# Kernel tuning notes

Hardware: AMD Instinct MI355X
Metric: run time of the kernel (lower is better)

Reference implementation:

```python
import jax, jax.numpy as jnp
import numpy as np

B, N, C, D, H = 256, 1024, 100, 256, 16
QD = D // H              # per-head dim
CLIP = 10.0              # logit_clipping
NEG = -1000000000.0      # masked_fill value in torch source


def setup_inputs() -> dict:
    key = jax.random.key(0)
    ks = jax.random.split(key, 12)
    s = 0.05
    inp = {
        "depot_embedding": jax.random.normal(ks[0], (B, 1, D), jnp.float32),
        "cluster_embedding": jax.random.normal(ks[1], (B, C + 1, D), jnp.float32),
        "current_embedding": jax.random.normal(ks[2], (B, 1, D), jnp.float32),
        "node_embeddings": jax.random.normal(ks[3], (B, N, D), jnp.float32),
        # visited-node / other-cluster / visited-cluster masks (bool)
        "mask": jax.random.bernoulli(ks[4], 0.2, (B, 1, N)),
        "cluster_mask": jax.random.bernoulli(ks[5], 0.5, (B, 1, N)),
        "visited_cluster_mask": jax.random.bernoulli(ks[6], 0.3, (B, 1, C + 1)).at[:, :, C].set(False),
        # Linear weights stored as (in, out) so y = x @ W
        "Wq": jax.random.normal(ks[7], (3 * D, D), jnp.float32) * s,
        "Wk": jax.random.normal(ks[8], (D, D), jnp.float32) * s,
        "Wv": jax.random.normal(ks[9], (D, D), jnp.float32) * s,
        "Wks": jax.random.normal(ks[10], (D, D), jnp.float32) * s,
        "Wo": jax.random.normal(ks[11], (D, D), jnp.float32) * s,
    }
    return inp


def _unvisited_mean(emb, m):
    # emb: [B,N,D], m: [B,1,N] bool -> masked mean over unvisited nodes [B,1,D]
    keep = (~m).astype(emb.dtype).transpose(0, 2, 1)          # [B,N,1]
    denom = jnp.clip(keep.sum(axis=1, keepdims=True), 1.0)    # [B,1,1]
    return (emb * keep).sum(axis=1, keepdims=True) / denom


def reference(depot_embedding, cluster_embedding, current_embedding,
              node_embeddings, mask, cluster_mask, visited_cluster_mask,
              Wq, Wk, Wv, Wks, Wo):
    b = node_embeddings.shape[0]
    # context query: [unvisited-mean, current, depot] -> [B,1,3D]
    uv = _unvisited_mean(node_embeddings, mask)
    context = jnp.concatenate([uv, current_embedding, depot_embedding], axis=-1)
    q = context @ Wq                    # [B,1,D]
    k = cluster_embedding @ Wk          # [B,C+1,D]
    v = cluster_embedding @ Wv
    prob_k = cluster_embedding @ Wks

    # visited-cluster mask; depot (col 0) only allowed once all real clusters visited
    vm = visited_cluster_mask[:, 0, :]                        # [B,C+1]
    all_real_visited = jnp.all(vm[:, 1:], axis=1)
    vm = vm.at[:, 0].set(~all_real_visited)

    # multi-head glimpse attention
    qh = q.reshape(b, 1, H, QD).transpose(0, 2, 1, 3)         # [B,H,1,QD]
    kh = k.reshape(b, -1, H, QD).transpose(0, 2, 1, 3)        # [B,H,C+1,QD]
    vh = v.reshape(b, -1, H, QD).transpose(0, 2, 1, 3)
    scores = jnp.einsum('bhqe,bhke->bhqk', qh, kh) / jnp.sqrt(jnp.float32(QD))
    scores = jnp.where(vm[:, None, None, :], NEG, scores)
    attn = jax.nn.softmax(scores, axis=-1)
    glimpse = jnp.einsum('bhqk,bhke->bhqe', attn, vh)
    glimpse = glimpse.transpose(0, 2, 1, 3).reshape(b, 1, D) @ Wo   # [B,1,D]

    # single-head pointer logits over clusters
    logits = jnp.einsum('bqd,bkd->bqk', glimpse, prob_k)[:, 0, :] / jnp.sqrt(jnp.float32(D))
    logits = jnp.tanh(logits) * CLIP
    logits = jnp.where(vm, NEG, logits)
    local_log_p = jax.nn.log_softmax(logits, axis=1)          # [B,C+1]

    # greedy cluster selection + gather
    selected_cluster = jnp.argmax(local_log_p, axis=1)        # [B] int
    sel_emb = jnp.take_along_axis(cluster_embedding,
                                  selected_cluster[:, None, None], axis=1)  # [B,1,D]

    uvc = _unvisited_mean(node_embeddings, mask | cluster_mask)
    init_aug = jnp.concatenate([uvc, current_embedding, sel_emb, depot_embedding], axis=-1)  # [B,1,4D]
    init_guidance_emb = sel_emb
    init_guidance = selected_cluster
    clu_prob = local_log_p
    return init_aug, init_guidance_emb, init_guidance, clu_prob
```

## Files before the change

### kernel.cpp

```cpp
#include <hip/hip_runtime.h>
#include <math.h>

#define B_SZ 256
#define N_SZ 1024
#define NCL  101
#define D_SZ 256
#define NH   16
#define APAD 260
#define NEGV (-1000000000.0f)


__device__ __forceinline__ bool mask_at(const void* p, long idx, int mode) {
  if (mode == 0) return ((const int*)p)[idx] != 0;
  if (mode == 1) return ((const unsigned char*)p)[idx] != 0;
  return ((const float*)p)[idx] != 0.0f;
}

__global__ void detect_mode_kernel(const unsigned int* m, int* flag) {
  if (threadIdx.x == 0 && blockIdx.x == 0) {
    bool isf = false, nonbin = false;
    for (int i = 0; i < 256; ++i) {
      unsigned int v = m[i];
      if (v == 0x3F800000u) isf = true;
      else if (v > 1u) nonbin = true;
    }
    *flag = isf ? 2 : (nonbin ? 1 : 0);
  }
}

__global__ __launch_bounds__(256) void mean_partial_kernel(
    const float* __restrict__ node, const void* __restrict__ mask,
    const void* __restrict__ cmask, const int* __restrict__ flag,
    int* __restrict__ counts, float* __restrict__ partials) {
  const int bs = blockIdx.x;
  const int b = bs >> 3, s = bs & 7;
  const int tid = threadIdx.x;
  const int mode = *flag;
  const int r0 = s * 128;
  __shared__ float f1[128], f2[128];
  __shared__ int wc1[2], wc2[2];
  __shared__ float red[4][D_SZ];

  int c1 = 0, c2 = 0;
  if (tid < 128) {
    const long idx = (long)b * N_SZ + r0 + tid;
    const bool m1 = mask_at(mask, idx, mode);
    const bool m2 = mask_at(cmask, idx, mode);
    const int k1 = m1 ? 0 : 1;
    const int k2 = (m1 || m2) ? 0 : 1;
    f1[tid] = (float)k1; f2[tid] = (float)k2;
    c1 = k1; c2 = k2;
  }
  #pragma unroll
  for (int off = 32; off > 0; off >>= 1) {
    c1 += __shfl_down(c1, off);
    c2 += __shfl_down(c2, off);
  }
  if (tid == 0)  { wc1[0] = c1; wc2[0] = c2; }
  if (tid == 64) { wc1[1] = c1; wc2[1] = c2; }
  __syncthreads();
  if (tid == 0) {
    counts[bs * 2 + 0] = wc1[0] + wc1[1];
    counts[bs * 2 + 1] = wc2[0] + wc2[1];
  }

  const int rg = tid >> 6;
  const int c4 = (tid & 63) << 2;
  const float* base = node + ((size_t)b * N_SZ + r0) * D_SZ + c4;
  float4 s1 = {0.f,0.f,0.f,0.f}, s2 = {0.f,0.f,0.f,0.f};
  #pragma unroll 8
  for (int k = 0; k < 32; ++k) {
    const int row = rg * 32 + k;
    const float4 x = *(const float4*)(base + (size_t)row * D_SZ);
    const float k1 = f1[row], k2 = f2[row];
    s1.x = fmaf(x.x, k1, s1.x); s1.y = fmaf(x.y, k1, s1.y);
    s1.z = fmaf(x.z, k1, s1.z); s1.w = fmaf(x.w, k1, s1.w);
    s2.x = fmaf(x.x, k2, s2.x); s2.y = fmaf(x.y, k2, s2.y);
    s2.z = fmaf(x.z, k2, s2.z); s2.w = fmaf(x.w, k2, s2.w);
  }
  *(float4*)&red[rg][c4] = s1;
  __syncthreads();
  {
    float t = red[0][tid] + red[1][tid] + red[2][tid] + red[3][tid];
    partials[((size_t)bs * 2 + 0) * D_SZ + tid] = t;
  }
  __syncthreads();
  *(float4*)&red[rg][c4] = s2;
  __syncthreads();
  {
    float t = red[0][tid] + red[1][tid] + red[2][tid] + red[3][tid];
    partials[((size_t)bs * 2 + 1) * D_SZ + tid] = t;
  }
}

struct __align__(16) SMem {
  float At[16][APAD];
  union { float tT[NH][APAD]; float uB[NH][APAD]; } tu;
  float sc[NH][104];
  float ctx[3 * D_SZ];
  float q[D_SZ];
  float g[D_SZ];
  float go[D_SZ];
  float w[D_SZ];
  float logits[104];
  int   vm[104];
  float lse_s;
  int   sel_s;
};

__global__ __launch_bounds__(256) void main_kernel(
    const float* __restrict__ depot, const float* __restrict__ cluster,
    const float* __restrict__ current, const void* __restrict__ vcm,
    const int* __restrict__ flag,
    const float* __restrict__ Wq, const float* __restrict__ Wk,
    const float* __restrict__ Wv, const float* __restrict__ Wks,
    const float* __restrict__ Wo,
    const int* __restrict__ counts, const float* __restrict__ partials,
    float* __restrict__ out) {
  __shared__ SMem S;
  const int b = blockIdx.x, tid = threadIdx.x;
  const int mode = *flag;
  const float* Ab = cluster + (size_t)b * NCL * D_SZ;

  float uvv = 0.f, uvcv = 0.f;
  #pragma unroll
  for (int s = 0; s < 8; ++s) {
    uvv  += partials[((size_t)(b * 8 + s) * 2 + 0) * D_SZ + tid];
    uvcv += partials[((size_t)(b * 8 + s) * 2 + 1) * D_SZ + tid];
  }
  int t1 = 0, t2 = 0;
  #pragma unroll
  for (int s = 0; s < 8; ++s) {
    t1 += counts[(b * 8 + s) * 2 + 0];
    t2 += counts[(b * 8 + s) * 2 + 1];
  }
  const float uvcval = uvcv / fmaxf((float)t2, 1.0f);

  if (tid < NCL) S.vm[tid] = mask_at(vcm, (long)b * NCL + tid, mode) ? 1 : 0;
  S.ctx[tid]       = uvv / fmaxf((float)t1, 1.0f);
  S.ctx[256 + tid] = current[b * D_SZ + tid];
  S.ctx[512 + tid] = depot[b * D_SZ + tid];
  __syncthreads();
  if (tid == 0) {
    int all1 = 1;
    for (int c = 1; c < NCL; ++c) all1 &= S.vm[c];
    S.vm[0] = all1 ? 0 : 1;
  }

  {
    float a0 = 0.f, a1 = 0.f, a2 = 0.f, a3 = 0.f;
    for (int i = 0; i < 3 * D_SZ; i += 4) {
      a0 = fmaf(S.ctx[i + 0], Wq[(size_t)(i + 0) * D_SZ + tid], a0);
      a1 = fmaf(S.ctx[i + 1], Wq[(size_t)(i + 1) * D_SZ + tid], a1);
      a2 = fmaf(S.ctx[i + 2], Wq[(size_t)(i + 2) * D_SZ + tid], a2);
      a3 = fmaf(S.ctx[i + 3], Wq[(size_t)(i + 3) * D_SZ + tid], a3);
    }
    S.q[tid] = (a0 + a1) + (a2 + a3);
  }
  __syncthreads();

  {
    const int h = tid & 15, i0 = tid >> 4;
    float qh[16];
    #pragma unroll
    for (int e = 0; e < 16; ++e) qh[e] = S.q[h * 16 + e];
    for (int k = 0; k < 16; ++k) {
      const int i = i0 + 16 * k;
      const float* wr = Wk + (size_t)i * D_SZ + h * 16;
      float acc = 0.f;
      #pragma unroll
      for (int e = 0; e < 16; ++e) acc = fmaf(wr[e], qh[e], acc);
      S.tu.tT[h][i] = acc;
    }
  }
  __syncthreads();

  for (int ch = 0; ch < 7; ++ch) {
    const int r0 = ch * 16;
    for (int x = tid; x < 16 * 64; x += 256) {
      const int r = x >> 6, cc = (x & 63) << 2;
      if (r0 + r < NCL) {
        const float4 v = *(const float4*)(Ab + (size_t)(r0 + r) * D_SZ + cc);
        *(float4*)&S.At[r][cc] = v;
      }
    }
    __syncthreads();
    {
      const int h = tid >> 4, cl = tid & 15, c = r0 + cl;
      float p0 = 0.f, p1 = 0.f, p2 = 0.f, p3 = 0.f;
      for (int i = 0; i < D_SZ; i += 4) {
        const float4 av = *(const float4*)&S.At[cl][i];
        const float4 tv = *(const float4*)&S.tu.tT[h][i];
        p0 = fmaf(av.x, tv.x, p0);
        p1 = fmaf(av.y, tv.y, p1);
        p2 = fmaf(av.z, tv.z, p2);
        p3 = fmaf(av.w, tv.w, p3);
      }
      if (c < NCL) {
        float sv = 0.25f * ((p0 + p1) + (p2 + p3));
        if (S.vm[c]) sv = NEGV;
        S.sc[h][c] = sv;
      }
    }
    __syncthreads();
  }

  {
    const int h = tid >> 4, j = tid & 15;
    float m = -3.0e38f;
    for (int c = j; c < NCL; c += 16) m = fmaxf(m, S.sc[h][c]);
    #pragma unroll
    for (int off = 8; off > 0; off >>= 1) m = fmaxf(m, __shfl_xor(m, off, 16));
    float ssum = 0.f;
    for (int c = j; c < NCL; c += 16) {
      const float e = expf(S.sc[h][c] - m);
      S.sc[h][c] = e;
      ssum += e;
    }
    #pragma unroll
    for (int off = 8; off > 0; off >>= 1) ssum += __shfl_xor(ssum, off, 16);
    const float inv = 1.0f / ssum;
    for (int c = j; c < NCL; c += 16) S.sc[h][c] *= inv;
  }
  __syncthreads();

  {
    float u[16];
    #pragma unroll
    for (int h = 0; h < 16; ++h) u[h] = 0.f;
    for (int ch = 0; ch < 7; ++ch) {
      const int r0 = ch * 16;
      for (int x = tid; x < 16 * 64; x += 256) {
        const int r = x >> 6, cc = (x & 63) << 2;
        if (r0 + r < NCL) {
          const float4 v = *(const float4*)(Ab + (size_t)(r0 + r) * D_SZ + cc);
          *(float4*)&S.At[r][cc] = v;
        }
      }
      __syncthreads();
      const int cmax = (NCL - r0 < 16) ? (NCL - r0) : 16;
      for (int cl = 0; cl < cmax; ++cl) {
        const float a = S.At[cl][tid];
        const int c = r0 + cl;
        #pragma unroll
        for (int h = 0; h < 16; ++h) u[h] = fmaf(S.sc[h][c], a, u[h]);
      }
      __syncthreads();
    }
    #pragma unroll
    for (int h = 0; h < 16; ++h) S.tu.uB[h][tid] = u[h];
  }
  __syncthreads();

  {
    const int h = tid >> 4;
    float p0 = 0.f, p1 = 0.f, p2 = 0.f, p3 = 0.f;
    for (int i = 0; i < D_SZ; i += 4) {
      p0 = fmaf(S.tu.uB[h][i + 0], Wv[(size_t)(i + 0) * D_SZ + tid], p0);
      p1 = fmaf(S.tu.uB[h][i + 1], Wv[(size_t)(i + 1) * D_SZ + tid], p1);
      p2 = fmaf(S.tu.uB[h][i + 2], Wv[(size_t)(i + 2) * D_SZ + tid], p2);
      p3 = fmaf(S.tu.uB[h][i + 3], Wv[(size_t)(i + 3) * D_SZ + tid], p3);
    }
    S.g[tid] = (p0 + p1) + (p2 + p3);
  }
  __syncthreads();

  {
    float p0 = 0.f, p1 = 0.f, p2 = 0.f, p3 = 0.f;
    for (int d = 0; d < D_SZ; d += 4) {
      p0 = fmaf(S.g[d + 0], Wo[(size_t)(d + 0) * D_SZ + tid], p0);
      p1 = fmaf(S.g[d + 1], Wo[(size_t)(d + 1) * D_SZ + tid], p1);
      p2 = fmaf(S.g[d + 2], Wo[(size_t)(d + 2) * D_SZ + tid], p2);
      p3 = fmaf(S.g[d + 3], Wo[(size_t)(d + 3) * D_SZ + tid], p3);
    }
    S.go[tid] = (p0 + p1) + (p2 + p3);
  }
  __syncthreads();

  {
    const float* wr = Wks + (size_t)tid * D_SZ;
    float p0 = 0.f, p1 = 0.f, p2 = 0.f, p3 = 0.f;
    for (int j = 0; j < D_SZ; j += 4) {
      const float4 w4 = *(const float4*)&wr[j];
      p0 = fmaf(w4.x, S.go[j + 0], p0);
      p1 = fmaf(w4.y, S.go[j + 1], p1);
      p2 = fmaf(w4.z, S.go[j + 2], p2);
      p3 = fmaf(w4.w, S.go[j + 3], p3);
    }
    S.w[tid] = (p0 + p1) + (p2 + p3);
  }
  __syncthreads();

  if (tid < NCL) {
    const float* ar = Ab + (size_t)tid * D_SZ;
    float p0 = 0.f, p1 = 0.f, p2 = 0.f, p3 = 0.f;
    for (int i = 0; i < D_SZ; i += 4) {
      const float4 a4 = *(const float4*)&ar[i];
      p0 = fmaf(a4.x, S.w[i + 0], p0);
      p1 = fmaf(a4.y, S.w[i + 1], p1);
      p2 = fmaf(a4.z, S.w[i + 2], p2);
      p3 = fmaf(a4.w, S.w[i + 3], p3);
    }
    float l = ((p0 + p1) + (p2 + p3)) * 0.0625f;
    l = tanhf(l) * 10.0f;
    if (S.vm[tid]) l = NEGV;
    S.logits[tid] = l;
  }
  __syncthreads();

  if (tid < 64) {
    float bv = -3.0e38f; int bi = 0;
    for (int c = tid; c < NCL; c += 64) {
      const float v = S.logits[c];
      if (v > bv) { bv = v; bi = c; }
    }
    #pragma unroll
    for (int off = 32; off > 0; off >>= 1) {
      const float ov = __shfl_xor(bv, off);
      const int   oi = __shfl_xor(bi, off);
      if (ov > bv || (ov == bv && oi < bi)) { bv = ov; bi = oi; }
    }
    float ss = 0.f;
    for (int c = tid; c < NCL; c += 64) ss += expf(S.logits[c] - bv);
    #pragma unroll
    for (int off = 32; off > 0; off >>= 1) ss += __shfl_xor(ss, off);
    if (tid == 0) { S.lse_s = bv + logf(ss); S.sel_s = bi; }
  }
  __syncthreads();

  const float lse = S.lse_s;
  const int sel = S.sel_s;
  if (tid < NCL) out[327936 + b * NCL + tid] = S.logits[tid] - lse;
  if (tid == 0)  out[327680 + b] = (float)sel;
  const float se = Ab[(size_t)sel * D_SZ + tid];
  out[262144 + b * D_SZ + tid] = se;
  float* ia = out + (size_t)b * 1024;
  ia[tid]       = uvcval;
  ia[256 + tid] = current[b * D_SZ + tid];
  ia[512 + tid] = se;
  ia[768 + tid] = depot[b * D_SZ + tid];
}

extern "C" void kernel_launch(void* const* d_in, const int* in_sizes, int n_in,
                              void* d_out, int out_size, void* d_ws, size_t ws_size,
                              hipStream_t stream) {
  const float* depot   = (const float*)d_in[0];
  const float* cluster = (const float*)d_in[1];
  const float* current = (const float*)d_in[2];
  const float* node    = (const float*)d_in[3];
  const void*  mask    = d_in[4];
  const void*  cmask   = d_in[5];
  const void*  vcm     = d_in[6];
  const float* Wq  = (const float*)d_in[7];
  const float* Wk  = (const float*)d_in[8];
  const float* Wv  = (const float*)d_in[9];
  const float* Wks = (const float*)d_in[10];
  const float* Wo  = (const float*)d_in[11];
  float* out = (float*)d_out;

  int*   flag     = (int*)d_ws;
  int*   counts   = (int*)((char*)d_ws + 1024);
  float* partials = (float*)((char*)d_ws + 1024 + 16384);

  hipLaunchKernelGGL(detect_mode_kernel, dim3(1), dim3(64), 0, stream,
                     (const unsigned int*)mask, flag);
  hipLaunchKernelGGL(mean_partial_kernel, dim3(B_SZ * 8), dim3(256), 0, stream,
                     node, mask, cmask, flag, counts, partials);
  hipLaunchKernelGGL(main_kernel, dim3(B_SZ), dim3(256), 0, stream,
                     depot, cluster, current, vcm, flag,
                     Wq, Wk, Wv, Wks, Wo, counts, partials, out);
}
```

Before: 499.3 us.

## Inline mask-mode detection and read cluster embeddings directly instead of staging in LDS

```diff
diff --git a/kernel.cpp b/kernel.cpp
--- a/kernel.cpp
+++ b/kernel.cpp
@@ -10,32 +10,31 @@
 #define NEGV (-1000000000.0f)
 
 
+__device__ __forceinline__ int detect_mode(const unsigned int* m) {
+  const int l = threadIdx.x & 63;
+  const uint4 w = ((const uint4*)m)[l];
+  const bool isf = (w.x == 0x3F800000u) || (w.y == 0x3F800000u) ||
+                   (w.z == 0x3F800000u) || (w.w == 0x3F800000u);
+  const bool big = (w.x > 1u) || (w.y > 1u) || (w.z > 1u) || (w.w > 1u);
+  const unsigned long long bf = __ballot(isf);
+  const unsigned long long bb = __ballot(big);
+  return bf ? 2 : (bb ? 1 : 0);
+}
+
 __device__ __forceinline__ bool mask_at(const void* p, long idx, int mode) {
   if (mode == 0) return ((const int*)p)[idx] != 0;
   if (mode == 1) return ((const unsigned char*)p)[idx] != 0;
   return ((const float*)p)[idx] != 0.0f;
 }
 
-__global__ void detect_mode_kernel(const unsigned int* m, int* flag) {
-  if (threadIdx.x == 0 && blockIdx.x == 0) {
-    bool isf = false, nonbin = false;
-    for (int i = 0; i < 256; ++i) {
-      unsigned int v = m[i];
-      if (v == 0x3F800000u) isf = true;
-      else if (v > 1u) nonbin = true;
-    }
-    *flag = isf ? 2 : (nonbin ? 1 : 0);
-  }
-}
-
 __global__ __launch_bounds__(256) void mean_partial_kernel(
     const float* __restrict__ node, const void* __restrict__ mask,
-    const void* __restrict__ cmask, const int* __restrict__ flag,
+    const void* __restrict__ cmask,
     int* __restrict__ counts, float* __restrict__ partials) {
   const int bs = blockIdx.x;
   const int b = bs >> 3, s = bs & 7;
   const int tid = threadIdx.x;
-  const int mode = *flag;
+  const int mode = detect_mode((const unsigned int*)mask);
   const int r0 = s * 128;
   __shared__ float f1[128], f2[128];
   __shared__ int wc1[2], wc2[2];
@@ -94,9 +93,9 @@
 }
 
 struct __align__(16) SMem {
-  float At[16][APAD];
   union { float tT[NH][APAD]; float uB[NH][APAD]; } tu;
   float sc[NH][104];
+  float scT[104][NH];
   float ctx[3 * D_SZ];
   float q[D_SZ];
   float g[D_SZ];
@@ -110,8 +109,8 @@
 
 __global__ __launch_bounds__(256) void main_kernel(
     const float* __restrict__ depot, const float* __restrict__ cluster,
-    const float* __restrict__ current, const void* __restrict__ vcm,
-    const int* __restrict__ flag,
+    const float* __restrict__ current, const void* __restrict__ mask,
+    const void* __restrict__ vcm,
     const float* __restrict__ Wq, const float* __restrict__ Wk,
     const float* __restrict__ Wv, const float* __restrict__ Wks,
     const float* __restrict__ Wo,
@@ -119,7 +118,7 @@
     float* __restrict__ out) {
   __shared__ SMem S;
   const int b = blockIdx.x, tid = threadIdx.x;
-  const int mode = *flag;
+  const int mode = detect_mode((const unsigned int*)mask);
   const float* Ab = cluster + (size_t)b * NCL * D_SZ;
 
   float uvv = 0.f, uvcv = 0.f;
@@ -175,26 +174,19 @@
   }
   __syncthreads();
 
-  for (int ch = 0; ch < 7; ++ch) {
-    const int r0 = ch * 16;
-    for (int x = tid; x < 16 * 64; x += 256) {
-      const int r = x >> 6, cc = (x & 63) << 2;
-      if (r0 + r < NCL) {
-        const float4 v = *(const float4*)(Ab + (size_t)(r0 + r) * D_SZ + cc);
-        *(float4*)&S.At[r][cc] = v;
-      }
-    }
-    __syncthreads();
-    {
-      const int h = tid >> 4, cl = tid & 15, c = r0 + cl;
+  {
+    const int h = tid >> 4, cl = tid & 15;
+    for (int k = 0; k < 7; ++k) {
+      const int c = k * 16 + cl;
+      const float* ar = Ab + (size_t)(c < NCL ? c : NCL - 1) * D_SZ;
       float p0 = 0.f, p1 = 0.f, p2 = 0.f, p3 = 0.f;
       for (int i = 0; i < D_SZ; i += 4) {
-        const float4 av = *(const float4*)&S.At[cl][i];
-        const float4 tv = *(const float4*)&S.tu.tT[h][i];
-        p0 = fmaf(av.x, tv.x, p0);
-        p1 = fmaf(av.y, tv.y, p1);
-        p2 = fmaf(av.z, tv.z, p2);
-        p3 = fmaf(av.w, tv.w, p3);
+        const float4 a4 = *(const float4*)(ar + i);
+        const float4 t4 = *(const float4*)&S.tu.tT[h][i];
+        p0 = fmaf(a4.x, t4.x, p0);
+        p1 = fmaf(a4.y, t4.y, p1);
+        p2 = fmaf(a4.z, t4.z, p2);
+        p3 = fmaf(a4.w, t4.w, p3);
       }
       if (c < NCL) {
         float sv = 0.25f * ((p0 + p1) + (p2 + p3));
@@ -202,8 +194,8 @@
         S.sc[h][c] = sv;
       }
     }
-    __syncthreads();
-  }
+  }
+  __syncthreads();
 
   {
     const int h = tid >> 4, j = tid & 15;
@@ -220,7 +212,7 @@
     #pragma unroll
     for (int off = 8; off > 0; off >>= 1) ssum += __shfl_xor(ssum, off, 16);
     const float inv = 1.0f / ssum;
-    for (int c = j; c < NCL; c += 16) S.sc[h][c] *= inv;
+    for (int c = j; c < NCL; c += 16) S.scT[c][h] = S.sc[h][c] * inv;
   }
   __syncthreads();
 
@@ -228,25 +220,22 @@
     float u[16];
     #pragma unroll
     for (int h = 0; h < 16; ++h) u[h] = 0.f;
-    for (int ch = 0; ch < 7; ++ch) {
-      const int r0 = ch * 16;
-      for (int x = tid; x < 16 * 64; x += 256) {
-        const int r = x >> 6, cc = (x & 63) << 2;
-        if (r0 + r < NCL) {
-          const float4 v = *(const float4*)(Ab + (size_t)(r0 + r) * D_SZ + cc);
-          *(float4*)&S.At[r][cc] = v;
-        }
-      }
-      __syncthreads();
-      const int cmax = (NCL - r0 < 16) ? (NCL - r0) : 16;
-      for (int cl = 0; cl < cmax; ++cl) {
-        const float a = S.At[cl][tid];
-        const int c = r0 + cl;
-        #pragma unroll
-        for (int h = 0; h < 16; ++h) u[h] = fmaf(S.sc[h][c], a, u[h]);
-      }
-      __syncthreads();
-    }
+    for (int c = 0; c < NCL; ++c) {
+      const float a = Ab[(size_t)c * D_SZ + tid];
+      const float4 w0 = *(const float4*)&S.scT[c][0];
+      const float4 w1 = *(const float4*)&S.scT[c][4];
+      const float4 w2 = *(const float4*)&S.scT[c][8];
+      const float4 w3 = *(const float4*)&S.scT[c][12];
+      u[0]  = fmaf(w0.x, a, u[0]);  u[1]  = fmaf(w0.y, a, u[1]);
+      u[2]  = fmaf(w0.z, a, u[2]);  u[3]  = fmaf(w0.w, a, u[3]);
+      u[4]  = fmaf(w1.x, a, u[4]);  u[5]  = fmaf(w1.y, a, u[5]);
+      u[6]  = fmaf(w1.z, a, u[6]);  u[7]  = fmaf(w1.w, a, u[7]);
+      u[8]  = fmaf(w2.x, a, u[8]);  u[9]  = fmaf(w2.y, a, u[9]);
+      u[10] = fmaf(w2.z, a, u[10]); u[11] = fmaf(w2.w, a, u[11]);
+      u[12] = fmaf(w3.x, a, u[12]); u[13] = fmaf(w3.y, a, u[13]);
+      u[14] = fmaf(w3.z, a, u[14]); u[15] = fmaf(w3.w, a, u[15]);
+    }
+    __syncthreads();
     #pragma unroll
     for (int h = 0; h < 16; ++h) S.tu.uB[h][tid] = u[h];
   }
@@ -358,15 +347,12 @@
   const float* Wo  = (const float*)d_in[11];
   float* out = (float*)d_out;
 
-  int*   flag     = (int*)d_ws;
-  int*   counts   = (int*)((char*)d_ws + 1024);
-  float* partials = (float*)((char*)d_ws + 1024 + 16384);
-
-  hipLaunchKernelGGL(detect_mode_kernel, dim3(1), dim3(64), 0, stream,
-                     (const unsigned int*)mask, flag);
+  int*   counts   = (int*)d_ws;
+  float* partials = (float*)((char*)d_ws + 16384);
+
   hipLaunchKernelGGL(mean_partial_kernel, dim3(B_SZ * 8), dim3(256), 0, stream,
-                     node, mask, cmask, flag, counts, partials);
+                     node, mask, cmask, counts, partials);
   hipLaunchKernelGGL(main_kernel, dim3(B_SZ), dim3(256), 0, stream,
-                     depot, cluster, current, vcm, flag,
+                     depot, cluster, current, mask, vcm,
                      Wq, Wk, Wv, Wks, Wo, counts, partials, out);
 }
```

After: 501.0 us. About the same (+0.3%).
